# Kernel optimization log

Measured on AMD Instinct MI355X. Metric: run time of the kernel, lower is better.

## Reference

```python
import jax, jax.numpy as jnp
import numpy as np

N = 100000   # nodes
E = 1000000  # edges
F = 64       # in_features == out_features
ALPHA = 0.2  # leaky-relu negative slope


def setup_inputs() -> dict:
    key = jax.random.key(0)
    k = jax.random.split(key, 6)
    h = jax.random.normal(k[0], (N, F), jnp.float32)
    W = jax.random.normal(k[1], (F, F), jnp.float32) * 0.1   # Linear weight [out,in]
    Wb = jnp.zeros((F,), jnp.float32)
    a = jax.random.normal(k[2], (2 * F,), jnp.float32) * 0.1  # attn vector (Linear(2F,1))
    ab = jnp.zeros((), jnp.float32)
    src = jax.random.randint(k[3], (E,), 0, N, dtype=jnp.int32)
    dst = jax.random.randint(k[4], (E,), 0, N, dtype=jnp.int32)
    return {"h": h, "W": W, "Wb": Wb, "a": a, "ab": ab, "src": src, "dst": dst}


def reference(h, W, Wb, a, ab, src, dst):
    # Wh = W(h)  (dropout is identity in eval mode / dropout=0)
    Wh = h @ W.T + Wb                                   # [N, F]
    # e = leakyrelu(a([Wh_src || Wh_dst])) ; split a to avoid concat
    a_src, a_dst = a[:F], a[F:]
    e = jax.nn.leaky_relu(Wh[src] @ a_src + Wh[dst] @ a_dst + ab, ALPHA)  # [E]
    # segment softmax over destination nodes (DGL mailbox softmax)
    m = jax.ops.segment_max(e, dst, num_segments=N)     # [N], -inf for empty
    m = jnp.where(jnp.isfinite(m), m, 0.0)
    ex = jnp.exp(e - m[dst])                            # [E]
    denom = jax.ops.segment_sum(ex, dst, num_segments=N)
    attn = ex / jnp.where(denom[dst] > 0, denom[dst], 1.0)
    # weighted scatter-sum of source features to destinations
    h_prime = jax.ops.segment_sum(attn[:, None] * Wh[src], dst, num_segments=N)  # [N, F]
    return h_prime
```

## Files before the change

kernel.cpp:

```cpp
#include <hip/hip_runtime.h>

#define NF 64
#define ALPHA 0.2f
#define BSH 7
#define BNODES 128
#define CAP 2048
#define PB 4096

typedef unsigned int  uint;
typedef unsigned short ushort;

typedef __attribute__((ext_vector_type(8))) short  short8;
typedef __attribute__((ext_vector_type(4))) float  floatx4;

__device__ __forceinline__ ushort f2bf(float x) {
    uint u = __float_as_uint(x);
    u += 0x7fffu + ((u >> 16) & 1u);
    return (ushort)(u >> 16);
}

__device__ __forceinline__ short8 pack8(float4 lo, float4 hi) {
    short8 r;
    r[0] = (short)f2bf(lo.x); r[1] = (short)f2bf(lo.y);
    r[2] = (short)f2bf(lo.z); r[3] = (short)f2bf(lo.w);
    r[4] = (short)f2bf(hi.x); r[5] = (short)f2bf(hi.y);
    r[6] = (short)f2bf(hi.z); r[7] = (short)f2bf(hi.w);
    return r;
}

__global__ __launch_bounds__(256) void wh_hist_kernel(
    const float* __restrict__ h, const float* __restrict__ W,
    const float* __restrict__ Wb, const float* __restrict__ a,
    ushort* __restrict__ whbf, float* __restrict__ s_src, float* __restrict__ s_dst,
    const int* __restrict__ dst, int* __restrict__ bcnt,
    int N, int E, int whB, int NB)
{
    __shared__ int lh[1024];
    int t = threadIdx.x;
    if ((int)blockIdx.x >= whB) {
        int base = ((int)blockIdx.x - whB) * PB;
        for (int i = t; i < 1024; i += 256) lh[i] = 0;
        __syncthreads();
        #pragma unroll
        for (int g = 0; g < 4; ++g) {
            int ei = base + g * 1024 + t * 4;
            if (ei + 3 < E) {
                int4 d4 = *(const int4*)&dst[ei];
                atomicAdd(&lh[d4.x >> BSH], 1); atomicAdd(&lh[d4.y >> BSH], 1);
                atomicAdd(&lh[d4.z >> BSH], 1); atomicAdd(&lh[d4.w >> BSH], 1);
            } else {
                for (int e = ei; e < E && e < ei + 4; ++e) atomicAdd(&lh[dst[e] >> BSH], 1);
            }
        }
        __syncthreads();
        for (int bb = t; bb < NB; bb += 256)
            if (lh[bb]) atomicAdd(&bcnt[bb], lh[bb]);
        return;
    }

    int lane = t & 63;
    int wave = t >> 6;
    int r0   = blockIdx.x * 64 + wave * 16;
    if (r0 >= N) return;
    int m    = lane & 15;
    int quad = lane >> 4;

    short8 bfrag[4][2];
    #pragma unroll
    for (int ct = 0; ct < 4; ++ct) {
        const float* wrow = W + (size_t)(ct * 16 + m) * 64 + quad * 8;
        #pragma unroll
        for (int kh = 0; kh < 2; ++kh) {
            float4 lo = *(const float4*)(wrow + kh * 32);
            float4 hi = *(const float4*)(wrow + kh * 32 + 4);
            bfrag[ct][kh] = pack8(lo, hi);
        }
    }

    int row_a = r0 + m; if (row_a >= N) row_a = N - 1;
    const float* hrow = h + (size_t)row_a * 64 + quad * 8;
    floatx4 zero = {0.f, 0.f, 0.f, 0.f};
    floatx4 acc[4] = {zero, zero, zero, zero};
    #pragma unroll
    for (int kh = 0; kh < 2; ++kh) {
        float4 lo = *(const float4*)(hrow + kh * 32);
        float4 hi = *(const float4*)(hrow + kh * 32 + 4);
        short8 af = pack8(lo, hi);
        #pragma unroll
        for (int ct = 0; ct < 4; ++ct)
            acc[ct] = __builtin_amdgcn_mfma_f32_16x16x32_bf16(af, bfrag[ct][kh], acc[ct], 0, 0, 0);
    }

    float p1[4] = {0.f, 0.f, 0.f, 0.f}, p2[4] = {0.f, 0.f, 0.f, 0.f};
    #pragma unroll
    for (int ct = 0; ct < 4; ++ct) {
        int col = ct * 16 + m;
        float wb  = Wb[col];
        float av1 = a[col];
        float av2 = a[64 + col];
        #pragma unroll
        for (int reg = 0; reg < 4; ++reg) {
            int row = r0 + quad * 4 + reg;
            float v = acc[ct][reg] + wb;
            if (row < N) whbf[(size_t)row * 64 + col] = f2bf(v);
            p1[reg] += v * av1;
            p2[reg] += v * av2;
        }
    }
    #pragma unroll
    for (int off = 8; off >= 1; off >>= 1) {
        #pragma unroll
        for (int reg = 0; reg < 4; ++reg) {
            p1[reg] += __shfl_down(p1[reg], off, 16);
            p2[reg] += __shfl_down(p2[reg], off, 16);
        }
    }
    if (m == 0) {
        #pragma unroll
        for (int reg = 0; reg < 4; ++reg) {
            int row = r0 + quad * 4 + reg;
            if (row < N) { s_src[row] = p1[reg]; s_dst[row] = p2[reg]; }
        }
    }
}

__global__ __launch_bounds__(256) void scan_buckets(
    const int* __restrict__ bcnt, int* __restrict__ bstart, int* __restrict__ bctr, int NB)
{
    __shared__ int s[256];
    int t = threadIdx.x;
    int v[16]; int loc = 0;
    #pragma unroll
    for (int i = 0; i < 16; ++i) {
        int idx = t * 16 + i;
        v[i] = (idx < NB) ? bcnt[idx] : 0;
        loc += v[i];
    }
    s[t] = loc; __syncthreads();
    for (int off = 1; off < 256; off <<= 1) {
        int x = (t >= off) ? s[t - off] : 0;
        __syncthreads();
        s[t] += x;
        __syncthreads();
    }
    int excl = s[t] - loc;
    #pragma unroll
    for (int i = 0; i < 16; ++i) {
        int idx = t * 16 + i;
        if (idx < NB) { bstart[idx] = excl; bctr[idx] = excl; }
        excl += v[i];
    }
    if (t == 255) bstart[NB] = excl;
}

__global__ __launch_bounds__(256) void partition_kernel(
    const int* __restrict__ src, const int* __restrict__ dst,
    int* __restrict__ bctr, uint* __restrict__ tmp, int E, int NB)
{
    __shared__ uint   stage[PB];
    __shared__ ushort bid[PB];
    __shared__ int    hist[1024];
    __shared__ int    lbase[1024];
    __shared__ int    ctr[1024];
    __shared__ int    gbase[1024];
    __shared__ int    sw[256];

    int t = threadIdx.x;
    int base = blockIdx.x * PB;
    int total = E - base; if (total > PB) total = PB; if (total < 0) total = 0;

    for (int i = t; i < 1024; i += 256) hist[i] = 0;
    __syncthreads();

    int vs[16], vd[16];
    #pragma unroll
    for (int g = 0; g < 4; ++g) {
        int ei = base + g * 1024 + t * 4;
        if (ei + 3 < E) {
            int4 s4 = *(const int4*)&src[ei];
            int4 d4 = *(const int4*)&dst[ei];
            vs[g*4+0]=s4.x; vs[g*4+1]=s4.y; vs[g*4+2]=s4.z; vs[g*4+3]=s4.w;
            vd[g*4+0]=d4.x; vd[g*4+1]=d4.y; vd[g*4+2]=d4.z; vd[g*4+3]=d4.w;
        } else {
            #pragma unroll
            for (int j = 0; j < 4; ++j) {
                int e = ei + j;
                vs[g*4+j] = (e < E) ? src[e] : -1;
                vd[g*4+j] = (e < E) ? dst[e] : -1;
            }
        }
    }
    #pragma unroll
    for (int i = 0; i < 16; ++i)
        if (vd[i] >= 0) atomicAdd(&hist[vd[i] >> BSH], 1);
    __syncthreads();

    int b0 = t * 4;
    int c0 = hist[b0], c1 = hist[b0+1], c2 = hist[b0+2], c3 = hist[b0+3];
    int tsum = c0 + c1 + c2 + c3;
    sw[t] = tsum; __syncthreads();
    for (int off = 1; off < 256; off <<= 1) {
        int x = (t >= off) ? sw[t - off] : 0;
        __syncthreads();
        sw[t] += x;
        __syncthreads();
    }
    int ex = sw[t] - tsum;
    lbase[b0] = ex;     ex += c0;
    lbase[b0+1] = ex;   ex += c1;
    lbase[b0+2] = ex;   ex += c2;
    lbase[b0+3] = ex;
    __syncthreads();

    for (int bb = t; bb < NB; bb += 256) {
        int c = hist[bb];
        gbase[bb] = c ? atomicAdd(&bctr[bb], c) : 0;
        ctr[bb] = lbase[bb];
    }
    __syncthreads();

    #pragma unroll
    for (int i = 0; i < 16; ++i) {
        int d = vd[i];
        if (d >= 0) {
            int bb = d >> BSH;
            int pos = atomicAdd(&ctr[bb], 1);
            stage[pos] = ((uint)vs[i] << BSH) | (uint)(d & (BNODES - 1));
            bid[pos] = (ushort)bb;
        }
    }
    __syncthreads();

    for (int i = t; i < total; i += 256) {
        int bb = bid[i];
        tmp[gbase[bb] + (i - lbase[bb])] = stage[i];
    }
}

__global__ __launch_bounds__(512) void bucket_aggregate(
    const uint* __restrict__ tmp, const int* __restrict__ bstart,
    const float* __restrict__ s_src, const float* __restrict__ s_dst,
    const float* __restrict__ ab, const ushort* __restrict__ whbf,
    float* __restrict__ out, int N)
{
    __shared__ uint  ssrc[CAP];
    __shared__ float sexv[CAP];
    __shared__ int   cnts[BNODES];
    __shared__ int   excl[BNODES + 1];
    __shared__ int   ctr[BNODES];
    __shared__ float sdl[BNODES];
    __shared__ int   sc[BNODES];

    int t = threadIdx.x;
    int b = blockIdx.x;
    int n0 = b << BSH;
    int lo = bstart[b], hi = bstart[b + 1];
    int cnt = hi - lo;
    float ab0 = ab[0];

    if (t < BNODES) {
        cnts[t] = 0;
        sdl[t] = (n0 + t < N) ? s_dst[n0 + t] + ab0 : 0.f;
    }
    __syncthreads();
    for (int i = t; i < cnt; i += 512)
        atomicAdd(&cnts[tmp[lo + i] & (BNODES - 1)], 1);
    __syncthreads();

    int v = (t < BNODES) ? cnts[t] : 0;
    if (t < BNODES) sc[t] = v;
    __syncthreads();
    for (int off = 1; off < BNODES; off <<= 1) {
        int x = (t < BNODES && t >= off) ? sc[t - off] : 0;
        __syncthreads();
        if (t < BNODES) sc[t] += x;
        __syncthreads();
    }
    if (t < BNODES) { excl[t] = sc[t] - v; ctr[t] = sc[t] - v; }
    if (t == BNODES - 1) excl[BNODES] = sc[BNODES - 1];
    __syncthreads();

    for (int i = t; i < cnt; i += 512) {
        uint val = tmp[lo + i];
        uint s = val >> BSH;
        int node = val & (BNODES - 1);
        float e = s_src[s] + sdl[node];
        e = e > 0.f ? e : ALPHA * e;
        float ex = __expf(e);
        int pos = atomicAdd(&ctr[node], 1);
        if (pos < CAP) { ssrc[pos] = s; sexv[pos] = ex; }
    }
    __syncthreads();

    int g = t >> 3, l8 = t & 7;
    int nlim = N - n0; if (nlim > BNODES) nlim = BNODES;
    for (int node = g; node < nlim; node += 64) {
        int e0 = excl[node];
        int e1 = excl[node + 1]; if (e1 > CAP) e1 = CAP;
        float f[8] = {0.f,0.f,0.f,0.f,0.f,0.f,0.f,0.f};
        float dn = 0.f;
        if (e0 < e1) {
            uint s = ssrc[e0]; float ev = sexv[e0];
            uint4 p = ((const uint4*)(whbf + (size_t)s * 64))[l8];
            for (int e = e0; e < e1; ++e) {
                int en = (e + 1 < e1) ? e + 1 : e0;
                uint sn = ssrc[en]; float evn = sexv[en];
                uint4 pn = ((const uint4*)(whbf + (size_t)sn * 64))[l8];
                f[0] += ev * __uint_as_float(p.x << 16);
                f[1] += ev * __uint_as_float(p.x & 0xffff0000u);
                f[2] += ev * __uint_as_float(p.y << 16);
                f[3] += ev * __uint_as_float(p.y & 0xffff0000u);
                f[4] += ev * __uint_as_float(p.z << 16);
                f[5] += ev * __uint_as_float(p.z & 0xffff0000u);
                f[6] += ev * __uint_as_float(p.w << 16);
                f[7] += ev * __uint_as_float(p.w & 0xffff0000u);
                dn += ev;
                s = sn; ev = evn; p = pn;
            }
        }
        float inv = dn > 0.f ? 1.f / dn : 1.f;
        float4 o0, o1;
        o0.x = f[0]*inv; o0.y = f[1]*inv; o0.z = f[2]*inv; o0.w = f[3]*inv;
        o1.x = f[4]*inv; o1.y = f[5]*inv; o1.z = f[6]*inv; o1.w = f[7]*inv;
        float* orow = out + (size_t)(n0 + node) * 64 + l8 * 8;
        *(float4*)orow       = o0;
        *(float4*)(orow + 4) = o1;
    }
}

extern "C" void kernel_launch(void* const* d_in, const int* in_sizes, int n_in,
                              void* d_out, int out_size, void* d_ws, size_t ws_size,
                              hipStream_t stream) {
    const float* h   = (const float*)d_in[0];
    const float* W   = (const float*)d_in[1];
    const float* Wb  = (const float*)d_in[2];
    const float* a   = (const float*)d_in[3];
    const float* ab  = (const float*)d_in[4];
    const int*   src = (const int*)d_in[5];
    const int*   dst = (const int*)d_in[6];

    int N = in_sizes[0] / NF;
    int E = in_sizes[5];
    float* out = (float*)d_out;
    int NB = (N + BNODES - 1) >> BSH;

    ushort* whbf   = (ushort*)d_ws;
    float*  s_src  = (float*)(whbf + (size_t)N * NF);
    float*  s_dst  = s_src + N;
    int*    bcnt   = (int*)(s_dst + N);
    int*    bstart = bcnt + NB;
    int*    bctr   = bstart + NB + 1;
    uint*   tmp    = (uint*)(bctr + NB);

    hipMemsetAsync(bcnt, 0, (size_t)NB * sizeof(int), stream);

    int whB   = (N + 63) / 64;
    int edgeB = (E + PB - 1) / PB;
    wh_hist_kernel<<<whB + edgeB, 256, 0, stream>>>(
        h, W, Wb, a, whbf, s_src, s_dst, dst, bcnt, N, E, whB, NB);

    scan_buckets<<<1, 256, 0, stream>>>(bcnt, bstart, bctr, NB);

    partition_kernel<<<edgeB, 256, 0, stream>>>(src, dst, bctr, tmp, E, NB);

    bucket_aggregate<<<NB, 512, 0, stream>>>(tmp, bstart, s_src, s_dst, ab, whbf, out, N);
}
```

Measured before the change: 157.0 us.

## Replace histogram+scan with fixed-capacity bucket slots and precompute edge exp in partition

Drops the separate dst histogram pass and the single-block scan kernel by giving each destination bucket a fixed CAPG-sized slot in the temp buffer, filled via atomic counters. The attention logit and its exp are now computed in the partition kernel and stored alongside the packed src/node pair as a uint2. The aggregate kernel then reads its bucket directly, uses a wave-shuffle scan and holds edges in registers. This removes one kernel launch, one full read of dst and a serial scan, at the cost of doubling temp-buffer traffic and silently dropping edges beyond CAPG per bucket. Random gather of s_src/s_dst also moves into partition.

Result: slower. 173.6 us (+10.6%).

```diff
diff --git a/kernel.cpp b/kernel.cpp
--- a/kernel.cpp
+++ b/kernel.cpp
@@ -4,7 +4,7 @@
 #define ALPHA 0.2f
 #define BSH 7
 #define BNODES 128
-#define CAP 2048
+#define CAPG 2048
 #define PB 4096
 
 typedef unsigned int  uint;
@@ -28,36 +28,13 @@
     return r;
 }
 
-__global__ __launch_bounds__(256) void wh_hist_kernel(
+__global__ __launch_bounds__(256) void wh_gemm_kernel(
     const float* __restrict__ h, const float* __restrict__ W,
     const float* __restrict__ Wb, const float* __restrict__ a,
     ushort* __restrict__ whbf, float* __restrict__ s_src, float* __restrict__ s_dst,
-    const int* __restrict__ dst, int* __restrict__ bcnt,
-    int N, int E, int whB, int NB)
+    int N)
 {
-    __shared__ int lh[1024];
     int t = threadIdx.x;
-    if ((int)blockIdx.x >= whB) {
-        int base = ((int)blockIdx.x - whB) * PB;
-        for (int i = t; i < 1024; i += 256) lh[i] = 0;
-        __syncthreads();
-        #pragma unroll
-        for (int g = 0; g < 4; ++g) {
-            int ei = base + g * 1024 + t * 4;
-            if (ei + 3 < E) {
-                int4 d4 = *(const int4*)&dst[ei];
-                atomicAdd(&lh[d4.x >> BSH], 1); atomicAdd(&lh[d4.y >> BSH], 1);
-                atomicAdd(&lh[d4.z >> BSH], 1); atomicAdd(&lh[d4.w >> BSH], 1);
-            } else {
-                for (int e = ei; e < E && e < ei + 4; ++e) atomicAdd(&lh[dst[e] >> BSH], 1);
-            }
-        }
-        __syncthreads();
-        for (int bb = t; bb < NB; bb += 256)
-            if (lh[bb]) atomicAdd(&bcnt[bb], lh[bb]);
-        return;
-    }
-
     int lane = t & 63;
     int wave = t >> 6;
     int r0   = blockIdx.x * 64 + wave * 16;
@@ -124,40 +101,13 @@
     }
 }
 
-__global__ __launch_bounds__(256) void scan_buckets(
-    const int* __restrict__ bcnt, int* __restrict__ bstart, int* __restrict__ bctr, int NB)
-{
-    __shared__ int s[256];
-    int t = threadIdx.x;
-    int v[16]; int loc = 0;
-    #pragma unroll
-    for (int i = 0; i < 16; ++i) {
-        int idx = t * 16 + i;
-        v[i] = (idx < NB) ? bcnt[idx] : 0;
-        loc += v[i];
-    }
-    s[t] = loc; __syncthreads();
-    for (int off = 1; off < 256; off <<= 1) {
-        int x = (t >= off) ? s[t - off] : 0;
-        __syncthreads();
-        s[t] += x;
-        __syncthreads();
-    }
-    int excl = s[t] - loc;
-    #pragma unroll
-    for (int i = 0; i < 16; ++i) {
-        int idx = t * 16 + i;
-        if (idx < NB) { bstart[idx] = excl; bctr[idx] = excl; }
-        excl += v[i];
-    }
-    if (t == 255) bstart[NB] = excl;
-}
-
 __global__ __launch_bounds__(256) void partition_kernel(
     const int* __restrict__ src, const int* __restrict__ dst,
-    int* __restrict__ bctr, uint* __restrict__ tmp, int E, int NB)
+    const float* __restrict__ s_src, const float* __restrict__ s_dst,
+    const float* __restrict__ ab,
+    int* __restrict__ bctr, uint2* __restrict__ tmp, int E, int NB)
 {
-    __shared__ uint   stage[PB];
+    __shared__ uint2  stage[PB];
     __shared__ ushort bid[PB];
     __shared__ int    hist[1024];
     __shared__ int    lbase[1024];
@@ -168,31 +118,42 @@
     int t = threadIdx.x;
     int base = blockIdx.x * PB;
     int total = E - base; if (total > PB) total = PB; if (total < 0) total = 0;
+    float ab0 = ab[0];
 
     for (int i = t; i < 1024; i += 256) hist[i] = 0;
     __syncthreads();
 
-    int vs[16], vd[16];
+    uint pk[16]; float ev[16]; int bb[16];
     #pragma unroll
     for (int g = 0; g < 4; ++g) {
         int ei = base + g * 1024 + t * 4;
+        int s4[4], d4[4];
         if (ei + 3 < E) {
-            int4 s4 = *(const int4*)&src[ei];
-            int4 d4 = *(const int4*)&dst[ei];
-            vs[g*4+0]=s4.x; vs[g*4+1]=s4.y; vs[g*4+2]=s4.z; vs[g*4+3]=s4.w;
-            vd[g*4+0]=d4.x; vd[g*4+1]=d4.y; vd[g*4+2]=d4.z; vd[g*4+3]=d4.w;
+            int4 sv = *(const int4*)&src[ei];
+            int4 dv = *(const int4*)&dst[ei];
+            s4[0]=sv.x; s4[1]=sv.y; s4[2]=sv.z; s4[3]=sv.w;
+            d4[0]=dv.x; d4[1]=dv.y; d4[2]=dv.z; d4[3]=dv.w;
         } else {
             #pragma unroll
             for (int j = 0; j < 4; ++j) {
                 int e = ei + j;
-                vs[g*4+j] = (e < E) ? src[e] : -1;
-                vd[g*4+j] = (e < E) ? dst[e] : -1;
+                s4[j] = (e < E) ? src[e] : -1;
+                d4[j] = (e < E) ? dst[e] : -1;
             }
         }
-    }
-    #pragma unroll
-    for (int i = 0; i < 16; ++i)
-        if (vd[i] >= 0) atomicAdd(&hist[vd[i] >> BSH], 1);
+        #pragma unroll
+        for (int j = 0; j < 4; ++j) {
+            int i16 = g * 4 + j;
+            if (d4[j] >= 0) {
+                float e = s_src[s4[j]] + s_dst[d4[j]] + ab0;
+                e = e > 0.f ? e : ALPHA * e;
+                ev[i16] = __expf(e);
+                pk[i16] = ((uint)s4[j] << BSH) | (uint)(d4[j] & (BNODES - 1));
+                bb[i16] = d4[j] >> BSH;
+                atomicAdd(&hist[bb[i16]], 1);
+            } else bb[i16] = -1;
+        }
+    }
     __syncthreads();
 
     int b0 = t * 4;
@@ -212,83 +173,82 @@
     lbase[b0+3] = ex;
     __syncthreads();
 
-    for (int bb = t; bb < NB; bb += 256) {
-        int c = hist[bb];
-        gbase[bb] = c ? atomicAdd(&bctr[bb], c) : 0;
-        ctr[bb] = lbase[bb];
+    for (int q = t; q < NB; q += 256) {
+        int c = hist[q];
+        gbase[q] = c ? atomicAdd(&bctr[q], c) : 0;
+        ctr[q] = lbase[q];
     }
     __syncthreads();
 
     #pragma unroll
     for (int i = 0; i < 16; ++i) {
-        int d = vd[i];
-        if (d >= 0) {
-            int bb = d >> BSH;
-            int pos = atomicAdd(&ctr[bb], 1);
-            stage[pos] = ((uint)vs[i] << BSH) | (uint)(d & (BNODES - 1));
-            bid[pos] = (ushort)bb;
+        if (bb[i] >= 0) {
+            int pos = atomicAdd(&ctr[bb[i]], 1);
+            stage[pos] = make_uint2(pk[i], __float_as_uint(ev[i]));
+            bid[pos] = (ushort)bb[i];
         }
     }
     __syncthreads();
 
     for (int i = t; i < total; i += 256) {
-        int bb = bid[i];
-        tmp[gbase[bb] + (i - lbase[bb])] = stage[i];
+        int q = bid[i];
+        int off = gbase[q] + (i - lbase[q]);
+        if (off < CAPG) tmp[(size_t)q * CAPG + off] = stage[i];
     }
 }
 
 __global__ __launch_bounds__(512) void bucket_aggregate(
-    const uint* __restrict__ tmp, const int* __restrict__ bstart,
-    const float* __restrict__ s_src, const float* __restrict__ s_dst,
-    const float* __restrict__ ab, const ushort* __restrict__ whbf,
-    float* __restrict__ out, int N)
+    const uint2* __restrict__ tmp, const int* __restrict__ bctr,
+    const ushort* __restrict__ whbf, float* __restrict__ out, int N)
 {
-    __shared__ uint  ssrc[CAP];
-    __shared__ float sexv[CAP];
+    __shared__ uint2 sed[CAPG];
     __shared__ int   cnts[BNODES];
     __shared__ int   excl[BNODES + 1];
     __shared__ int   ctr[BNODES];
-    __shared__ float sdl[BNODES];
-    __shared__ int   sc[BNODES];
 
     int t = threadIdx.x;
     int b = blockIdx.x;
     int n0 = b << BSH;
-    int lo = bstart[b], hi = bstart[b + 1];
-    int cnt = hi - lo;
-    float ab0 = ab[0];
-
-    if (t < BNODES) {
-        cnts[t] = 0;
-        sdl[t] = (n0 + t < N) ? s_dst[n0 + t] + ab0 : 0.f;
-    }
-    __syncthreads();
-    for (int i = t; i < cnt; i += 512)
-        atomicAdd(&cnts[tmp[lo + i] & (BNODES - 1)], 1);
-    __syncthreads();
-
-    int v = (t < BNODES) ? cnts[t] : 0;
-    if (t < BNODES) sc[t] = v;
-    __syncthreads();
-    for (int off = 1; off < BNODES; off <<= 1) {
-        int x = (t < BNODES && t >= off) ? sc[t - off] : 0;
-        __syncthreads();
-        if (t < BNODES) sc[t] += x;
-        __syncthreads();
-    }
-    if (t < BNODES) { excl[t] = sc[t] - v; ctr[t] = sc[t] - v; }
-    if (t == BNODES - 1) excl[BNODES] = sc[BNODES - 1];
-    __syncthreads();
-
-    for (int i = t; i < cnt; i += 512) {
-        uint val = tmp[lo + i];
-        uint s = val >> BSH;
-        int node = val & (BNODES - 1);
-        float e = s_src[s] + sdl[node];
-        e = e > 0.f ? e : ALPHA * e;
-        float ex = __expf(e);
-        int pos = atomicAdd(&ctr[node], 1);
-        if (pos < CAP) { ssrc[pos] = s; sexv[pos] = ex; }
+    int cnt = bctr[b]; if (cnt > CAPG) cnt = CAPG;
+
+    if (t < BNODES) cnts[t] = 0;
+    __syncthreads();
+
+    uint2 held[4]; int nh = 0;
+    #pragma unroll
+    for (int j = 0; j < 4; ++j) {
+        int idx = t + j * 512;
+        if (idx < cnt) {
+            uint2 v = tmp[(size_t)b * CAPG + idx];
+            held[nh++] = v;
+            atomicAdd(&cnts[v.x & (BNODES - 1)], 1);
+        }
+    }
+    __syncthreads();
+
+    if (t < 64) {
+        int c0 = cnts[2*t], c1 = cnts[2*t+1];
+        int s = c0 + c1;
+        int incl = s;
+        #pragma unroll
+        for (int off = 1; off < 64; off <<= 1) {
+            int x = __shfl_up(incl, off, 64);
+            if (t >= off) incl += x;
+        }
+        int e0 = incl - s;
+        excl[2*t] = e0;          ctr[2*t] = e0;
+        excl[2*t+1] = e0 + c0;   ctr[2*t+1] = e0 + c0;
+        if (t == 63) excl[BNODES] = incl;
+    }
+    __syncthreads();
+
+    #pragma unroll
+    for (int j = 0; j < 4; ++j) {
+        if (j < nh) {
+            uint2 v = held[j];
+            int pos = atomicAdd(&ctr[v.x & (BNODES - 1)], 1);
+            sed[pos] = v;
+        }
     }
     __syncthreads();
 
@@ -296,26 +256,28 @@
     int nlim = N - n0; if (nlim > BNODES) nlim = BNODES;
     for (int node = g; node < nlim; node += 64) {
         int e0 = excl[node];
-        int e1 = excl[node + 1]; if (e1 > CAP) e1 = CAP;
+        int e1 = excl[node + 1];
         float f[8] = {0.f,0.f,0.f,0.f,0.f,0.f,0.f,0.f};
         float dn = 0.f;
         if (e0 < e1) {
-            uint s = ssrc[e0]; float ev = sexv[e0];
+            uint2 v = sed[e0];
+            uint s = v.x >> BSH; float evv = __uint_as_float(v.y);
             uint4 p = ((const uint4*)(whbf + (size_t)s * 64))[l8];
             for (int e = e0; e < e1; ++e) {
                 int en = (e + 1 < e1) ? e + 1 : e0;
-                uint sn = ssrc[en]; float evn = sexv[en];
+                uint2 vn = sed[en];
+                uint sn = vn.x >> BSH; float evn = __uint_as_float(vn.y);
                 uint4 pn = ((const uint4*)(whbf + (size_t)sn * 64))[l8];
-                f[0] += ev * __uint_as_float(p.x << 16);
-                f[1] += ev * __uint_as_float(p.x & 0xffff0000u);
-                f[2] += ev * __uint_as_float(p.y << 16);
-                f[3] += ev * __uint_as_float(p.y & 0xffff0000u);
-                f[4] += ev * __uint_as_float(p.z << 16);
-                f[5] += ev * __uint_as_float(p.z & 0xffff0000u);
-                f[6] += ev * __uint_as_float(p.w << 16);
-                f[7] += ev * __uint_as_float(p.w & 0xffff0000u);
-                dn += ev;
-                s = sn; ev = evn; p = pn;
+                f[0] += evv * __uint_as_float(p.x << 16);
+                f[1] += evv * __uint_as_float(p.x & 0xffff0000u);
+                f[2] += evv * __uint_as_float(p.y << 16);
+                f[3] += evv * __uint_as_float(p.y & 0xffff0000u);
+                f[4] += evv * __uint_as_float(p.z << 16);
+                f[5] += evv * __uint_as_float(p.z & 0xffff0000u);
+                f[6] += evv * __uint_as_float(p.w << 16);
+                f[7] += evv * __uint_as_float(p.w & 0xffff0000u);
+                dn += evv;
+                evv = evn; p = pn;
             }
         }
         float inv = dn > 0.f ? 1.f / dn : 1.f;
@@ -347,21 +309,17 @@
     ushort* whbf   = (ushort*)d_ws;
     float*  s_src  = (float*)(whbf + (size_t)N * NF);
     float*  s_dst  = s_src + N;
-    int*    bcnt   = (int*)(s_dst + N);
-    int*    bstart = bcnt + NB;
-    int*    bctr   = bstart + NB + 1;
-    uint*   tmp    = (uint*)(bctr + NB);
-
-    hipMemsetAsync(bcnt, 0, (size_t)NB * sizeof(int), stream);
+    int*    bctr   = (int*)(s_dst + N);
+    uint2*  tmp    = (uint2*)(bctr + NB);
+
+    hipMemsetAsync(bctr, 0, (size_t)NB * sizeof(int), stream);
 
     int whB   = (N + 63) / 64;
     int edgeB = (E + PB - 1) / PB;
-    wh_hist_kernel<<<whB + edgeB, 256, 0, stream>>>(
-        h, W, Wb, a, whbf, s_src, s_dst, dst, bcnt, N, E, whB, NB);
-
-    scan_buckets<<<1, 256, 0, stream>>>(bcnt, bstart, bctr, NB);
-
-    partition_kernel<<<edgeB, 256, 0, stream>>>(src, dst, bctr, tmp, E, NB);
-
-    bucket_aggregate<<<NB, 512, 0, stream>>>(tmp, bstart, s_src, s_dst, ab, whbf, out, N);
-}
+
+    wh_gemm_kernel<<<whB, 256, 0, stream>>>(h, W, Wb, a, whbf, s_src, s_dst, N);
+
+    partition_kernel<<<edgeB, 256, 0, stream>>>(src, dst, s_src, s_dst, ab, bctr, tmp, E, NB);
+
+    bucket_aggregate<<<NB, 512, 0, stream>>>(tmp, bctr, whbf, out, N);
+}
```
